# Optimization experiments

Hardware: AMD Instinct MI355X
Metric: run time of the kernel (lower is better)

The kernel has to match this reference:

```python
import jax, jax.numpy as jnp
import numpy as np

HID = (128, 256, 128)  # nmp_qc NNet hidden layer sizes
D_IN = 256
TARGET = 256


def _mlp_params(key, n_in, n_out, prefix):
    sizes = (n_in,) + HID + (n_out,)
    params = {}
    for i in range(len(sizes) - 1):
        key, k1, k2 = jax.random.split(key, 3)
        fan_in = sizes[i]
        bound = 1.0 / np.sqrt(fan_in)
        params[f"{prefix}_W{i}"] = jax.random.uniform(k1, (sizes[i], sizes[i + 1]), jnp.float32, -bound, bound)
        params[f"{prefix}_b{i}"] = jax.random.uniform(k2, (sizes[i + 1],), jnp.float32, -bound, bound)
    return params, key


def _mlp(x, Ws, bs):
    # ReLU on all layers except the last (linear output), matching NNet
    for i in range(len(Ws) - 1):
        x = jax.nn.relu(x @ Ws[i] + bs[i])
    return x @ Ws[-1] + bs[-1]


def setup_inputs() -> dict:
    key = jax.random.key(0)
    k0, k1, key = jax.random.split(key, 3)
    B, N = 512, 256
    inp = {
        "h0": jax.random.normal(k0, (B, N, D_IN), jnp.float32),
        "hT": jax.random.normal(k1, (B, N, D_IN), jnp.float32),
    }
    gp, key = _mlp_params(key, 2 * D_IN, TARGET, "g")  # gate MLP: concat(h0,hT) -> target
    op, key = _mlp_params(key, D_IN, TARGET, "o")      # value MLP: hT -> target
    inp.update(gp)
    inp.update(op)
    return inp


def reference(h0, hT,
              g_W0, g_b0, g_W1, g_b1, g_W2, g_b2, g_W3, g_b3,
              o_W0, o_b0, o_W1, o_b1, o_W2, o_b2, o_W3, o_b3):
    gWs = (g_W0, g_W1, g_W2, g_W3)
    gbs = (g_b0, g_b1, g_b2, g_b3)
    oWs = (o_W0, o_W1, o_W2, o_W3)
    obs = (o_b0, o_b1, o_b2, o_b3)
    # gate: sigmoid(MLP1([h0; hT])) ; value: MLP2(hT)  -- all [B, N, target]
    gate = jax.nn.sigmoid(_mlp(jnp.concatenate([h0, hT], axis=-1), gWs, gbs))
    val = _mlp(hT, oWs, obs)
    # node validity mask: sum of initial features > 0, matching r_mpnn
    mask = (jnp.sum(h0, axis=-1, keepdims=True) > 0).astype(h0.dtype)  # [B, N, 1]
    return jnp.sum(mask * gate * val, axis=1)  # [B, target]
```

## Files before the change

### kernel.cpp

```cpp
#include <hip/hip_runtime.h>
#include <hip/hip_bf16.h>
#include <stdint.h>


typedef __attribute__((ext_vector_type(8))) short short8_t;
typedef __attribute__((ext_vector_type(16))) float f32x16;

#define ROWS 64
#define NWG  2048
#define NTHR 512

#define PE        (64 * 136)
#define OFF_P     0
#define OFF_A     34816
#define OFF_MASK  52224
#define LDS_TOTAL 52480

__device__ __forceinline__ short f2bf(float f) {
  union { float f; uint32_t u; } v; v.f = f;
  uint32_t r = (v.u + 0x7FFFu + ((v.u >> 16) & 1u)) >> 16;
  return (short)r;
}
__device__ __forceinline__ float bf2f(short b) {
  union { uint32_t u; float f; } v; v.u = ((uint32_t)(uint16_t)b) << 16;
  return v.f;
}

template <int KT16, int KSTEPS, int CT>
__device__ __forceinline__ void gemm32(const short* actin, int Sin,
                                       const short* __restrict__ wsB, int ks0, int cb0,
                                       f32x16 (&acc)[CT], int lane) {
  const int n32 = lane & 31, q32 = lane >> 5;
#pragma unroll
  for (int ks = 0; ks < KSTEPS; ++ks) {
    const int kl = ks * 16 + q32 * 8;
    short8_t b[CT];
#pragma unroll
    for (int ct = 0; ct < CT; ++ct)
      b[ct] = *(const short8_t*)(wsB + (((cb0 + ct) * KT16 + ks0 + ks) << 9) + lane * 8);
    const short8_t a = *(const short8_t*)(actin + n32 * Sin + kl);
#pragma unroll
    for (int ct = 0; ct < CT; ++ct)
      acc[ct] = __builtin_amdgcn_mfma_f32_32x32x16_bf16(a, b[ct], acc[ct], 0, 0, 0);
  }
}

template <int CT, int ACTF>
__device__ __forceinline__ void epi32(f32x16 (&acc)[CT], short* actout, int Sout,
                                      const float* __restrict__ bias, int c0, int n32, int q32) {
#pragma unroll
  for (int ct = 0; ct < CT; ++ct) {
    const int c = c0 + ct * 32 + n32;
    const float bv = bias[c];
#pragma unroll
    for (int reg = 0; reg < 16; ++reg) {
      const int r = (reg & 3) + 8 * (reg >> 2) + 4 * q32;
      float v = acc[ct][reg] + bv;
      if (ACTF == 1) v = fmaxf(v, 0.f);
      actout[r * Sout + c] = f2bf(v);
    }
  }
}

template <int K, int N, int ACTF>
__device__ __forceinline__ void layer32(const short* actin, int Sin, short* actout, int Sout,
                                        const short* __restrict__ wsB,
                                        const float* __restrict__ bias,
                                        int wq, int lane) {
  constexpr int CT = N / 128;
  const int cb0 = wq * CT;
  const int n32 = lane & 31, q32 = lane >> 5;
  f32x16 acc[CT];
#pragma unroll
  for (int ct = 0; ct < CT; ++ct) acc[ct] = (f32x16)(0.f);
  gemm32<K / 16, K / 16, CT>(actin, Sin, wsB, 0, cb0, acc, lane);
  epi32<CT, ACTF>(acc, actout, Sout, bias, cb0 * 32, n32, q32);
}

__device__ __forceinline__ void stage_load(const float* __restrict__ src, int row0, int colbase,
                                           int tid, float4 (&v)[4]) {
  const int c4 = tid & 31, rb = tid >> 5;
#pragma unroll
  for (int it = 0; it < 4; ++it)
    v[it] = *(const float4*)(src + (size_t)(row0 + rb + it * 16) * 256 + colbase + c4 * 4);
}

__device__ __forceinline__ void stage_store(short* Pb, int tid, const float4 (&v)[4],
                                            float* maskacc, int mmode) {
  const int c4 = tid & 31, rb = tid >> 5;
#pragma unroll
  for (int it = 0; it < 4; ++it) {
    const int r = rb + it * 16;
    short4 pk; pk.x = f2bf(v[it].x); pk.y = f2bf(v[it].y); pk.z = f2bf(v[it].z); pk.w = f2bf(v[it].w);
    *(short4*)(Pb + r * 136 + c4 * 4) = pk;
    if (mmode) {
      float s = v[it].x + v[it].y + v[it].z + v[it].w;
      s += __shfl_down(s, 16, 32);
      s += __shfl_down(s, 8, 32);
      s += __shfl_down(s, 4, 32);
      s += __shfl_down(s, 2, 32);
      s += __shfl_down(s, 1, 32);
      if (c4 == 0) {
        if (mmode == 1) maskacc[r] = s; else maskacc[r] += s;
      }
    }
  }
}

template <int NCH, bool MASKA>
__device__ __forceinline__ void stream32(const float* __restrict__ src0,
                                         const float* __restrict__ src1, int splitc,
                                         const short* __restrict__ wsB,
                                         const float* __restrict__ bias,
                                         short* P, short* Aout, float* maskacc,
                                         int row0, int tid, int wq, int rowsh, int lane) {
  constexpr int KT16 = NCH * 8;
  const int n32 = lane & 31, q32 = lane >> 5;
  f32x16 acc[1];
  acc[0] = (f32x16)(0.f);
  float4 v[4];
  stage_load(src0, row0, 0, tid, v);
  stage_store(P, tid, v, maskacc, MASKA ? 1 : 0);
  __syncthreads();
#pragma unroll
  for (int kc = 0; kc < NCH; ++kc) {
    if (kc + 1 < NCH) {
      const bool lo = (kc + 1 < splitc);
      stage_load(lo ? src0 : src1, row0, (lo ? kc + 1 : kc + 1 - splitc) * 128, tid, v);
    }
    gemm32<KT16, 8, 1>(P + (kc & 1) * PE + rowsh, 136, wsB, kc * 8, wq, acc, lane);
    if (kc + 1 < NCH)
      stage_store(P + ((kc + 1) & 1) * PE, tid, v, maskacc, (MASKA && kc + 1 < splitc) ? 2 : 0);
    __syncthreads();
  }
  epi32<1, 1>(acc, Aout, 136, bias, wq * 32, n32, q32);
}

__device__ __forceinline__ void gate_layer(const short* actin, const short* __restrict__ wsB,
                                           const float* __restrict__ bias,
                                           uint32_t (&gate)[2][8],
                                           int wq, int lane) {
  const int n32 = lane & 31;
  f32x16 acc[2];
  acc[0] = (f32x16)(0.f); acc[1] = (f32x16)(0.f);
  gemm32<8, 8, 2>(actin, 136, wsB, 0, wq * 2, acc, lane);
#pragma unroll
  for (int ct = 0; ct < 2; ++ct) {
    const float bv = bias[wq * 64 + ct * 32 + n32];
#pragma unroll
    for (int p = 0; p < 8; ++p) {
      const float g0 = 1.f / (1.f + __expf(-(acc[ct][2 * p] + bv)));
      const float g1 = 1.f / (1.f + __expf(-(acc[ct][2 * p + 1] + bv)));
      gate[ct][p] = ((uint32_t)(uint16_t)f2bf(g1) << 16) | (uint32_t)(uint16_t)f2bf(g0);
    }
  }
}

__device__ __forceinline__ void final32(const short* actin, const short* __restrict__ wsB,
                                        const float* __restrict__ bias,
                                        const uint32_t (&gate)[2][8],
                                        const float* maskacc, float* __restrict__ out,
                                        int row0, int wq, int lane) {
  const int n32 = lane & 31, q32 = lane >> 5;
  f32x16 acc[2];
  acc[0] = (f32x16)(0.f); acc[1] = (f32x16)(0.f);
  gemm32<8, 8, 2>(actin, 136, wsB, 0, wq * 2, acc, lane);

  const int b = row0 >> 8;
#pragma unroll
  for (int ct = 0; ct < 2; ++ct) {
    const int c = wq * 64 + ct * 32 + n32;
    const float bv = bias[c];
    float s = 0.f;
#pragma unroll
    for (int p = 0; p < 8; ++p) {
      const int r0 = ((2 * p) & 3) + 8 * (p >> 1) + 4 * q32;
      const float g0 = bf2f((short)(gate[ct][p] & 0xFFFF));
      const float g1 = bf2f((short)(gate[ct][p] >> 16));
      const float v0 = acc[ct][2 * p] + bv;
      const float v1 = acc[ct][2 * p + 1] + bv;
      if (maskacc[r0] > 0.f)     s += g0 * v0;
      if (maskacc[r0 + 1] > 0.f) s += g1 * v1;
    }
    s += __shfl_down(s, 32);
    if (lane < 32) atomicAdd(out + b * 256 + c, s);
  }
}

__global__ __launch_bounds__(NTHR, 6)
void readout_main(const float* __restrict__ h0, const float* __restrict__ hT,
                  const short* __restrict__ ws,
                  const float* __restrict__ gb0, const float* __restrict__ gb1,
                  const float* __restrict__ gb2, const float* __restrict__ gb3,
                  const float* __restrict__ ob0, const float* __restrict__ ob1,
                  const float* __restrict__ ob2, const float* __restrict__ ob3,
                  float* __restrict__ out) {
  __shared__ __align__(16) char smem[LDS_TOTAL];
  short* P  = (short*)(smem + OFF_P);
  short* B2 = (short*)(smem + OFF_P);
  short* A  = (short*)(smem + OFF_A);
  float* maskacc = (float*)(smem + OFF_MASK);

  const int tid = threadIdx.x, lane = tid & 63, wv = tid >> 6;
  const int wq = wv & 3;
  const int rhalf = wv >> 2;
  const int rsh136 = rhalf * 32 * 136;
  const int rsh264 = rhalf * 32 * 264;
  const int row0 = blockIdx.x * ROWS;
  uint32_t gate[2][8];

  stream32<4, true>(h0, hT, 2, ws + 0, gb0, P, A + rsh136, maskacc, row0, tid, wq, rsh136, lane);
  __syncthreads();
  layer32<128, 256, 1>(A + rsh136, 136, B2 + rsh264, 264, ws + 65536, gb1, wq, lane);
  __syncthreads();
  layer32<256, 128, 1>(B2 + rsh264, 264, A + rsh136, 136, ws + 98304, gb2, wq, lane);
  __syncthreads();
  gate_layer(A + rsh136, ws + 131072, gb3, gate, wq, lane);
  __syncthreads();
  stream32<2, false>(hT, hT, 2, ws + 163840, ob0, P, A + rsh136, maskacc, row0, tid, wq, rsh136, lane);
  __syncthreads();
  layer32<128, 256, 1>(A + rsh136, 136, B2 + rsh264, 264, ws + 196608, ob1, wq, lane);
  __syncthreads();
  layer32<256, 128, 1>(B2 + rsh264, 264, A + rsh136, 136, ws + 229376, ob2, wq, lane);
  __syncthreads();
  final32(A + rsh136, ws + 262144, ob3, gate, maskacc + rhalf * 32, out, row0, wq, lane);
}

__global__ void prep(const float* __restrict__ W0, const float* __restrict__ W1,
                     const float* __restrict__ W2, const float* __restrict__ W3,
                     const float* __restrict__ W4, const float* __restrict__ W5,
                     const float* __restrict__ W6, const float* __restrict__ W7,
                     short* __restrict__ ws, float* __restrict__ out) {
  const int l = blockIdx.y;
  const int le = blockIdx.x * 256 + threadIdx.x;
  if (l == 1) { out[le] = 0.f; out[le + 65536] = 0.f; }
  int K, N, off; const float* W;
  switch (l) {
    case 0:  K = 512; N = 128; off = 0;      W = W0; break;
    case 1:  K = 128; N = 256; off = 65536;  W = W1; break;
    case 2:  K = 256; N = 128; off = 98304;  W = W2; break;
    case 3:  K = 128; N = 256; off = 131072; W = W3; break;
    case 4:  K = 256; N = 128; off = 163840; W = W4; break;
    case 5:  K = 128; N = 256; off = 196608; W = W5; break;
    case 6:  K = 256; N = 128; off = 229376; W = W6; break;
    default: K = 128; N = 256; off = 262144; W = W7; break;
  }
  if (le >= K * N) return;
  const int j = le & 7;
  const int lanei = (le >> 3) & 63;
  const int blk = le >> 9;
  const int kt16 = K >> 4;
  const int ks = blk % kt16, cb = blk / kt16;
  const int n = cb * 32 + (lanei & 31);
  const int k = ks * 16 + (lanei >> 5) * 8 + j;
  ws[off + le] = f2bf(W[k * N + n]);
}

extern "C" void kernel_launch(void* const* d_in, const int* in_sizes, int n_in,
                              void* d_out, int out_size, void* d_ws, size_t ws_size,
                              hipStream_t stream) {
  const float* h0  = (const float*)d_in[0];
  const float* hT  = (const float*)d_in[1];
  const float* gW0 = (const float*)d_in[2];  const float* gb0 = (const float*)d_in[3];
  const float* gW1 = (const float*)d_in[4];  const float* gb1 = (const float*)d_in[5];
  const float* gW2 = (const float*)d_in[6];  const float* gb2 = (const float*)d_in[7];
  const float* gW3 = (const float*)d_in[8];  const float* gb3 = (const float*)d_in[9];
  const float* oW0 = (const float*)d_in[10]; const float* ob0 = (const float*)d_in[11];
  const float* oW1 = (const float*)d_in[12]; const float* ob1 = (const float*)d_in[13];
  const float* oW2 = (const float*)d_in[14]; const float* ob2 = (const float*)d_in[15];
  const float* oW3 = (const float*)d_in[16]; const float* ob3 = (const float*)d_in[17];
  float* out = (float*)d_out;
  short* ws  = (short*)d_ws;

  prep<<<dim3(256, 8), 256, 0, stream>>>(gW0, gW1, gW2, gW3, oW0, oW1, oW2, oW3, ws, out);
  readout_main<<<NWG, NTHR, 0, stream>>>(h0, hT, ws,
                                         gb0, gb1, gb2, gb3,
                                         ob0, ob1, ob2, ob3, out);
}
```

Before: 429.7 us.

## Halve workgroup to 4 waves, each covering all 64 rows with two row tiles

The workgroup shrinks from 8 waves to 4. Each wave now computes two 32-row MFMA tiles per 32-column block, so one weight fragment is reused across both row tiles instead of being loaded by two row-halves. The wide hidden layer is split into two 128-column halves fused with the following layer's K-accumulation (mid_pair), which drops the 264-stride buffer and shrinks LDS. Staging is now single-buffered, with a load then sync then compute per chunk, so the previous double-buffered prefetch overlap is lost. Launch bounds drop to 4 waves per SIMD occupancy hint.

```diff
diff --git a/kernel.cpp b/kernel.cpp
--- a/kernel.cpp
+++ b/kernel.cpp
@@ -8,13 +8,12 @@
 
 #define ROWS 64
 #define NWG  2048
-#define NTHR 512
-
-#define PE        (64 * 136)
+#define NTHR 256
+
 #define OFF_P     0
-#define OFF_A     34816
-#define OFF_MASK  52224
-#define LDS_TOTAL 52480
+#define OFF_A     17408
+#define OFF_MASK  34816
+#define LDS_TOTAL 35072
 
 __device__ __forceinline__ short f2bf(float f) {
   union { float f; uint32_t u; } v; v.f = f;
@@ -26,71 +25,53 @@
   return v.f;
 }
 
-template <int KT16, int KSTEPS, int CT>
+template <int KT16, int KSTEPS>
 __device__ __forceinline__ void gemm32(const short* actin, int Sin,
-                                       const short* __restrict__ wsB, int ks0, int cb0,
-                                       f32x16 (&acc)[CT], int lane) {
+                                       const short* __restrict__ wsB, int ks0, int cb,
+                                       f32x16 (&acc)[2], int lane) {
   const int n32 = lane & 31, q32 = lane >> 5;
 #pragma unroll
   for (int ks = 0; ks < KSTEPS; ++ks) {
     const int kl = ks * 16 + q32 * 8;
-    short8_t b[CT];
-#pragma unroll
-    for (int ct = 0; ct < CT; ++ct)
-      b[ct] = *(const short8_t*)(wsB + (((cb0 + ct) * KT16 + ks0 + ks) << 9) + lane * 8);
-    const short8_t a = *(const short8_t*)(actin + n32 * Sin + kl);
-#pragma unroll
-    for (int ct = 0; ct < CT; ++ct)
-      acc[ct] = __builtin_amdgcn_mfma_f32_32x32x16_bf16(a, b[ct], acc[ct], 0, 0, 0);
-  }
-}
-
-template <int CT, int ACTF>
-__device__ __forceinline__ void epi32(f32x16 (&acc)[CT], short* actout, int Sout,
-                                      const float* __restrict__ bias, int c0, int n32, int q32) {
-#pragma unroll
-  for (int ct = 0; ct < CT; ++ct) {
-    const int c = c0 + ct * 32 + n32;
-    const float bv = bias[c];
+    const short8_t b = *(const short8_t*)(wsB + ((cb * KT16 + ks0 + ks) << 9) + lane * 8);
+    short8_t a[2];
+#pragma unroll
+    for (int rt = 0; rt < 2; ++rt)
+      a[rt] = *(const short8_t*)(actin + (rt * 32 + n32) * Sin + kl);
+#pragma unroll
+    for (int rt = 0; rt < 2; ++rt)
+      acc[rt] = __builtin_amdgcn_mfma_f32_32x32x16_bf16(a[rt], b, acc[rt], 0, 0, 0);
+  }
+}
+
+template <int ACTF>
+__device__ __forceinline__ void epi32(f32x16 (&acc)[2], short* actout, int Sout,
+                                      const float* __restrict__ bias, int c0,
+                                      int n32, int q32) {
+  const int c = c0 + n32;
+  const float bv = bias[c];
+#pragma unroll
+  for (int rt = 0; rt < 2; ++rt)
 #pragma unroll
     for (int reg = 0; reg < 16; ++reg) {
-      const int r = (reg & 3) + 8 * (reg >> 2) + 4 * q32;
-      float v = acc[ct][reg] + bv;
+      const int r = rt * 32 + (reg & 3) + 8 * (reg >> 2) + 4 * q32;
+      float v = acc[rt][reg] + bv;
       if (ACTF == 1) v = fmaxf(v, 0.f);
       actout[r * Sout + c] = f2bf(v);
     }
-  }
-}
-
-template <int K, int N, int ACTF>
-__device__ __forceinline__ void layer32(const short* actin, int Sin, short* actout, int Sout,
-                                        const short* __restrict__ wsB,
-                                        const float* __restrict__ bias,
-                                        int wq, int lane) {
-  constexpr int CT = N / 128;
-  const int cb0 = wq * CT;
-  const int n32 = lane & 31, q32 = lane >> 5;
-  f32x16 acc[CT];
-#pragma unroll
-  for (int ct = 0; ct < CT; ++ct) acc[ct] = (f32x16)(0.f);
-  gemm32<K / 16, K / 16, CT>(actin, Sin, wsB, 0, cb0, acc, lane);
-  epi32<CT, ACTF>(acc, actout, Sout, bias, cb0 * 32, n32, q32);
-}
-
-__device__ __forceinline__ void stage_load(const float* __restrict__ src, int row0, int colbase,
-                                           int tid, float4 (&v)[4]) {
+}
+
+__device__ __forceinline__ void stage_half(const float* __restrict__ src, int row0,
+                                           int colbase, int rowoff, short* Pb,
+                                           float* maskacc, int mmode, int tid) {
   const int c4 = tid & 31, rb = tid >> 5;
+  float4 v[4];
 #pragma unroll
   for (int it = 0; it < 4; ++it)
-    v[it] = *(const float4*)(src + (size_t)(row0 + rb + it * 16) * 256 + colbase + c4 * 4);
-}
-
-__device__ __forceinline__ void stage_store(short* Pb, int tid, const float4 (&v)[4],
-                                            float* maskacc, int mmode) {
-  const int c4 = tid & 31, rb = tid >> 5;
+    v[it] = *(const float4*)(src + (size_t)(row0 + rowoff + rb + it * 8) * 256 + colbase + c4 * 4);
 #pragma unroll
   for (int it = 0; it < 4; ++it) {
-    const int r = rb + it * 16;
+    const int r = rowoff + rb + it * 8;
     short4 pk; pk.x = f2bf(v[it].x); pk.y = f2bf(v[it].y); pk.z = f2bf(v[it].z); pk.w = f2bf(v[it].w);
     *(short4*)(Pb + r * 136 + c4 * 4) = pk;
     if (mmode) {
@@ -112,82 +93,106 @@
                                          const float* __restrict__ src1, int splitc,
                                          const short* __restrict__ wsB,
                                          const float* __restrict__ bias,
-                                         short* P, short* Aout, float* maskacc,
-                                         int row0, int tid, int wq, int rowsh, int lane) {
+                                         short* P, short* A, float* maskacc,
+                                         int row0, int tid, int wq, int lane) {
   constexpr int KT16 = NCH * 8;
   const int n32 = lane & 31, q32 = lane >> 5;
-  f32x16 acc[1];
-  acc[0] = (f32x16)(0.f);
-  float4 v[4];
-  stage_load(src0, row0, 0, tid, v);
-  stage_store(P, tid, v, maskacc, MASKA ? 1 : 0);
+  f32x16 acc[2];
+  acc[0] = (f32x16)(0.f); acc[1] = (f32x16)(0.f);
+#pragma unroll
+  for (int kc = 0; kc < NCH; ++kc) {
+    const bool lo = (kc < splitc);
+    const float* src = lo ? src0 : src1;
+    const int colbase = (lo ? kc : kc - splitc) * 128;
+    const int mm = MASKA ? (kc == 0 ? 1 : (lo ? 2 : 0)) : 0;
+    stage_half(src, row0, colbase, 0,  P, maskacc, mm, tid);
+    stage_half(src, row0, colbase, 32, P, maskacc, mm, tid);
+    __syncthreads();
+    gemm32<KT16, 8>(P, 136, wsB, kc * 8, wq, acc, lane);
+    __syncthreads();
+  }
+  epi32<1>(acc, A, 136, bias, wq * 32, n32, q32);
   __syncthreads();
-#pragma unroll
-  for (int kc = 0; kc < NCH; ++kc) {
-    if (kc + 1 < NCH) {
-      const bool lo = (kc + 1 < splitc);
-      stage_load(lo ? src0 : src1, row0, (lo ? kc + 1 : kc + 1 - splitc) * 128, tid, v);
-    }
-    gemm32<KT16, 8, 1>(P + (kc & 1) * PE + rowsh, 136, wsB, kc * 8, wq, acc, lane);
-    if (kc + 1 < NCH)
-      stage_store(P + ((kc + 1) & 1) * PE, tid, v, maskacc, (MASKA && kc + 1 < splitc) ? 2 : 0);
-    __syncthreads();
-  }
-  epi32<1, 1>(acc, Aout, 136, bias, wq * 32, n32, q32);
-}
-
-__device__ __forceinline__ void gate_layer(const short* actin, const short* __restrict__ wsB,
+}
+
+__device__ __forceinline__ void mid_pair(short* A, short* P,
+                                         const short* __restrict__ ws1,
+                                         const float* __restrict__ b1,
+                                         const short* __restrict__ ws2,
+                                         const float* __restrict__ b2,
+                                         int wq, int lane) {
+  const int n32 = lane & 31, q32 = lane >> 5;
+  f32x16 acc2[2];
+  acc2[0] = (f32x16)(0.f); acc2[1] = (f32x16)(0.f);
+#pragma unroll
+  for (int h = 0; h < 2; ++h) {
+    f32x16 acc1[2];
+    acc1[0] = (f32x16)(0.f); acc1[1] = (f32x16)(0.f);
+    gemm32<8, 8>(A, 136, ws1, 0, h * 4 + wq, acc1, lane);
+    epi32<1>(acc1, P, 136, b1 + h * 128, wq * 32, n32, q32);
+    __syncthreads();
+    gemm32<16, 8>(P, 136, ws2, h * 8, wq, acc2, lane);
+    __syncthreads();
+  }
+  epi32<1>(acc2, A, 136, b2, wq * 32, n32, q32);
+  __syncthreads();
+}
+
+__device__ __forceinline__ void gate_layer(const short* A, const short* __restrict__ wsB,
                                            const float* __restrict__ bias,
-                                           uint32_t (&gate)[2][8],
+                                           uint32_t (&gate)[2][2][8],
                                            int wq, int lane) {
   const int n32 = lane & 31;
-  f32x16 acc[2];
-  acc[0] = (f32x16)(0.f); acc[1] = (f32x16)(0.f);
-  gemm32<8, 8, 2>(actin, 136, wsB, 0, wq * 2, acc, lane);
-#pragma unroll
-  for (int ct = 0; ct < 2; ++ct) {
-    const float bv = bias[wq * 64 + ct * 32 + n32];
-#pragma unroll
-    for (int p = 0; p < 8; ++p) {
-      const float g0 = 1.f / (1.f + __expf(-(acc[ct][2 * p] + bv)));
-      const float g1 = 1.f / (1.f + __expf(-(acc[ct][2 * p + 1] + bv)));
-      gate[ct][p] = ((uint32_t)(uint16_t)f2bf(g1) << 16) | (uint32_t)(uint16_t)f2bf(g0);
-    }
-  }
-}
-
-__device__ __forceinline__ void final32(const short* actin, const short* __restrict__ wsB,
+#pragma unroll
+  for (int h = 0; h < 2; ++h) {
+    f32x16 acc[2];
+    acc[0] = (f32x16)(0.f); acc[1] = (f32x16)(0.f);
+    gemm32<8, 8>(A, 136, wsB, 0, h * 4 + wq, acc, lane);
+    const float bv = bias[h * 128 + wq * 32 + n32];
+#pragma unroll
+    for (int rt = 0; rt < 2; ++rt)
+#pragma unroll
+      for (int p = 0; p < 8; ++p) {
+        const float g0 = 1.f / (1.f + __expf(-(acc[rt][2 * p] + bv)));
+        const float g1 = 1.f / (1.f + __expf(-(acc[rt][2 * p + 1] + bv)));
+        gate[rt][h][p] = ((uint32_t)(uint16_t)f2bf(g1) << 16) | (uint32_t)(uint16_t)f2bf(g0);
+      }
+  }
+}
+
+__device__ __forceinline__ void final32(const short* A, const short* __restrict__ wsB,
                                         const float* __restrict__ bias,
-                                        const uint32_t (&gate)[2][8],
+                                        const uint32_t (&gate)[2][2][8],
                                         const float* maskacc, float* __restrict__ out,
                                         int row0, int wq, int lane) {
   const int n32 = lane & 31, q32 = lane >> 5;
-  f32x16 acc[2];
-  acc[0] = (f32x16)(0.f); acc[1] = (f32x16)(0.f);
-  gemm32<8, 8, 2>(actin, 136, wsB, 0, wq * 2, acc, lane);
-
   const int b = row0 >> 8;
 #pragma unroll
-  for (int ct = 0; ct < 2; ++ct) {
-    const int c = wq * 64 + ct * 32 + n32;
+  for (int h = 0; h < 2; ++h) {
+    f32x16 acc[2];
+    acc[0] = (f32x16)(0.f); acc[1] = (f32x16)(0.f);
+    gemm32<8, 8>(A, 136, wsB, 0, h * 4 + wq, acc, lane);
+    const int c = h * 128 + wq * 32 + n32;
     const float bv = bias[c];
     float s = 0.f;
 #pragma unroll
-    for (int p = 0; p < 8; ++p) {
-      const int r0 = ((2 * p) & 3) + 8 * (p >> 1) + 4 * q32;
-      const float g0 = bf2f((short)(gate[ct][p] & 0xFFFF));
-      const float g1 = bf2f((short)(gate[ct][p] >> 16));
-      const float v0 = acc[ct][2 * p] + bv;
-      const float v1 = acc[ct][2 * p + 1] + bv;
-      if (maskacc[r0] > 0.f)     s += g0 * v0;
-      if (maskacc[r0 + 1] > 0.f) s += g1 * v1;
-    }
+    for (int rt = 0; rt < 2; ++rt)
+#pragma unroll
+      for (int p = 0; p < 8; ++p) {
+        const int r0 = rt * 32 + ((2 * p) & 3) + 8 * (p >> 1) + 4 * q32;
+        const float g0 = bf2f((short)(gate[rt][h][p] & 0xFFFF));
+        const float g1 = bf2f((short)(gate[rt][h][p] >> 16));
+        const float v0 = acc[rt][2 * p] + bv;
+        const float v1 = acc[rt][2 * p + 1] + bv;
+        if (maskacc[r0] > 0.f)     s += g0 * v0;
+        if (maskacc[r0 + 1] > 0.f) s += g1 * v1;
+      }
     s += __shfl_down(s, 32);
     if (lane < 32) atomicAdd(out + b * 256 + c, s);
   }
 }
 
-__global__ __launch_bounds__(NTHR, 6)
+__global__ __launch_bounds__(NTHR, 4)
 void readout_main(const float* __restrict__ h0, const float* __restrict__ hT,
                   const short* __restrict__ ws,
                   const float* __restrict__ gb0, const float* __restrict__ gb1,
@@ -197,33 +202,19 @@
                   float* __restrict__ out) {
   __shared__ __align__(16) char smem[LDS_TOTAL];
   short* P  = (short*)(smem + OFF_P);
-  short* B2 = (short*)(smem + OFF_P);
   short* A  = (short*)(smem + OFF_A);
   float* maskacc = (float*)(smem + OFF_MASK);
 
-  const int tid = threadIdx.x, lane = tid & 63, wv = tid >> 6;
-  const int wq = wv & 3;
-  const int rhalf = wv >> 2;
-  const int rsh136 = rhalf * 32 * 136;
-  const int rsh264 = rhalf * 32 * 264;
+  const int tid = threadIdx.x, lane = tid & 63, wq = tid >> 6;
   const int row0 = blockIdx.x * ROWS;
-  uint32_t gate[2][8];
-
-  stream32<4, true>(h0, hT, 2, ws + 0, gb0, P, A + rsh136, maskacc, row0, tid, wq, rsh136, lane);
-  __syncthreads();
-  layer32<128, 256, 1>(A + rsh136, 136, B2 + rsh264, 264, ws + 65536, gb1, wq, lane);
-  __syncthreads();
-  layer32<256, 128, 1>(B2 + rsh264, 264, A + rsh136, 136, ws + 98304, gb2, wq, lane);
-  __syncthreads();
-  gate_layer(A + rsh136, ws + 131072, gb3, gate, wq, lane);
-  __syncthreads();
-  stream32<2, false>(hT, hT, 2, ws + 163840, ob0, P, A + rsh136, maskacc, row0, tid, wq, rsh136, lane);
-  __syncthreads();
-  layer32<128, 256, 1>(A + rsh136, 136, B2 + rsh264, 264, ws + 196608, ob1, wq, lane);
-  __syncthreads();
-  layer32<256, 128, 1>(B2 + rsh264, 264, A + rsh136, 136, ws + 229376, ob2, wq, lane);
-  __syncthreads();
-  final32(A + rsh136, ws + 262144, ob3, gate, maskacc + rhalf * 32, out, row0, wq, lane);
+  uint32_t gate[2][2][8];
+
+  stream32<4, true>(h0, hT, 2, ws + 0, gb0, P, A, maskacc, row0, tid, wq, lane);
+  mid_pair(A, P, ws + 65536, gb1, ws + 98304, gb2, wq, lane);
+  gate_layer(A, ws + 131072, gb3, gate, wq, lane);
+  stream32<2, false>(hT, hT, 2, ws + 163840, ob0, P, A, maskacc, row0, tid, wq, lane);
+  mid_pair(A, P, ws + 196608, ob1, ws + 229376, ob2, wq, lane);
+  final32(A, ws + 262144, ob3, gate, maskacc, out, row0, wq, lane);
 }
 
 __global__ void prep(const float* __restrict__ W0, const float* __restrict__ W1,
```

Result: slower. 450.9 us (+4.9%).
